# Performance work log

Hardware: AMD Instinct MI355X
Metric: run time of the kernel (lower is better)

Reference implementation:

```python
import jax, jax.numpy as jnp
import numpy as np

EPS = 1e-5

def _layernorm(x, g, b):
    mu = jnp.mean(x, axis=-1, keepdims=True)
    var = jnp.mean(jnp.square(x - mu), axis=-1, keepdims=True)
    return (x - mu) * jax.lax.rsqrt(var + EPS) * g + b

def _mlp(x, w1, b1, w2, b2):
    h = jax.nn.gelu(jnp.einsum('bnd,dh->bnh', x, w1) + b1, approximate=False)
    return jnp.einsum('bnh,hd->bnd', h, w2) + b2

def setup_inputs() -> dict:
    key = jax.random.key(0)
    B, N, D, H = 2, 8192, 1024, 4096
    ks = jax.random.split(key, 12)
    s1 = 1.0 / np.sqrt(D)
    s2 = 1.0 / np.sqrt(H)
    return {
        'x': jax.random.normal(ks[0], (B, N, D), dtype=jnp.float32),
        'mask': jax.random.randint(ks[1], (B, N), 0, 2) > 0,
        'g_rgb': jnp.ones((D,), jnp.float32),
        'b_rgb': jnp.zeros((D,), jnp.float32),
        'w1_rgb': jax.random.normal(ks[2], (D, H), dtype=jnp.float32) * s1,
        'b1_rgb': jnp.zeros((H,), jnp.float32),
        'w2_rgb': jax.random.normal(ks[3], (H, D), dtype=jnp.float32) * s2,
        'b2_rgb': jnp.zeros((D,), jnp.float32),
        'g_expr': jnp.ones((D,), jnp.float32),
        'b_expr': jnp.zeros((D,), jnp.float32),
        'w1_expr': jax.random.normal(ks[4], (D, H), dtype=jnp.float32) * s1,
        'b1_expr': jnp.zeros((H,), jnp.float32),
        'w2_expr': jax.random.normal(ks[5], (H, D), dtype=jnp.float32) * s2,
        'b2_expr': jnp.zeros((D,), jnp.float32),
    }

def reference(x, mask, g_rgb, b_rgb, w1_rgb, b1_rgb, w2_rgb, b2_rgb,
              g_expr, b_expr, w1_expr, b1_expr, w2_expr, b2_expr):
    # Per-token routing: rgb expert where mask, expr expert where ~mask.
    # LayerNorm+MLP are pointwise per token, so dense compute + select is
    # mathematically identical to the torch gather->compute->scatter.
    z_rgb = _mlp(_layernorm(x, g_rgb, b_rgb), w1_rgb, b1_rgb, w2_rgb, b2_rgb)
    z_expr = _mlp(_layernorm(x, g_expr, b_expr), w1_expr, b1_expr, w2_expr, b2_expr)
    z = jnp.where(mask[..., None], z_rgb, z_expr)
    return z.astype(jnp.float16)  # torch scatters into a float16 buffer
```

## Files before the change

kernel.cpp:

```cpp
#include <hip/hip_runtime.h>
#include <hip/hip_bf16.h>
#include <hip/hip_fp16.h>

#define D_ 1024
#define H_ 4096
#define NTOK 16384
#define MPAD 16640

typedef __attribute__((ext_vector_type(8))) short bf16x8;
typedef __attribute__((ext_vector_type(4))) float f32x4;

static __device__ __forceinline__ unsigned short f2bf(float f) {
  union { float f; unsigned u; } x; x.f = f;
  unsigned u = x.u + 0x7fffu + ((x.u >> 16) & 1u);
  return (unsigned short)(u >> 16);
}

static __device__ __forceinline__ void gld16(const void* g, void* l) {
  __builtin_amdgcn_global_load_lds(
      (const __attribute__((address_space(1))) unsigned int*)g,
      (__attribute__((address_space(3))) unsigned int*)l, 16, 0, 0);
}

static __device__ __forceinline__ float gelu_fast(float x) {
  const float z = x * (1.5957691216f + 0.0713548163f * x * x);
  return x * __builtin_amdgcn_rcpf(1.0f + __expf(-z));
}

__global__ __launch_bounds__(256) void transpose4_kernel(
    const float* __restrict__ w1r, const float* __restrict__ w1e,
    const float* __restrict__ w2r, const float* __restrict__ w2e,
    unsigned short* __restrict__ o1r, unsigned short* __restrict__ o1e,
    unsigned short* __restrict__ o2r, unsigned short* __restrict__ o2e) {
  __shared__ float tile[32][33];
  const int t = blockIdx.x;
  const float* src; unsigned short* dst; int R, C, tl;
  if (t < 4096)       { src = w1r; dst = o1r; R = D_; C = H_; tl = t; }
  else if (t < 8192)  { src = w1e; dst = o1e; R = D_; C = H_; tl = t - 4096; }
  else if (t < 12288) { src = w2r; dst = o2r; R = H_; C = D_; tl = t - 8192; }
  else                { src = w2e; dst = o2e; R = H_; C = D_; tl = t - 12288; }
  const int tc = C >> 5;
  const int r0 = (tl / tc) * 32, c0 = (tl % tc) * 32;
  const int tx = threadIdx.x & 31, ty = threadIdx.x >> 5;
#pragma unroll
  for (int i = 0; i < 32; i += 8)
    tile[ty + i][tx] = src[(size_t)(r0 + ty + i) * C + c0 + tx];
  __syncthreads();
#pragma unroll
  for (int i = 0; i < 32; i += 8)
    dst[(size_t)(c0 + ty + i) * R + r0 + tx] = f2bf(tile[tx][ty + i]);
}

__global__ __launch_bounds__(256) void compact_kernel(
    const int* __restrict__ mask, int* __restrict__ perm, int* __restrict__ counts) {
  const int NT = 256, CH = NTOK / NT;
  __shared__ int sm[NTOK];
  __shared__ int wsum[4];
  const int t = threadIdx.x;
  const int ln = t & 63, wv = t >> 6;
  for (int i = t; i < NTOK; i += NT) sm[i] = mask[i];
  for (int i = t; i < MPAD; i += NT) perm[i] = -1;
  __syncthreads();
  const int base = t * CH;
  int cnt = 0;
  for (int i = 0; i < CH; ++i) cnt += (sm[base + i] != 0);
  int sc = cnt;
#pragma unroll
  for (int o = 1; o < 64; o <<= 1) {
    int u = __shfl_up(sc, o, 64);
    if (ln >= o) sc += u;
  }
  if (ln == 63) wsum[wv] = sc;
  __syncthreads();
  int woff = 0;
#pragma unroll
  for (int j = 0; j < 4; ++j) woff += (j < wv) ? wsum[j] : 0;
  const int total1 = wsum[0] + wsum[1] + wsum[2] + wsum[3];
  if (t == 0) { counts[0] = total1; counts[1] = NTOK - total1; }
  const int excl = woff + sc - cnt;
  const int expr_base = ((total1 + 255) >> 8) << 8;
  int p1 = excl;
  int p0 = expr_base + (base - excl);
  for (int i = 0; i < CH; ++i) {
    const int idx = base + i;
    if (sm[idx] != 0) perm[p1++] = idx; else perm[p0++] = idx;
  }
}

__global__ __launch_bounds__(256) void ln_kernel(
    const float* __restrict__ x, const int* __restrict__ mask,
    const int* __restrict__ perm,
    const float* __restrict__ g_rgb, const float* __restrict__ b_rgb,
    const float* __restrict__ g_expr, const float* __restrict__ b_expr,
    unsigned short* __restrict__ xln) {
  const int i = blockIdx.x;
  const int t = perm[i];
  if (t < 0) return;
  const int tid = threadIdx.x;
  const float4 v = ((const float4*)(x + (size_t)t * D_))[tid];
  float s = v.x + v.y + v.z + v.w;
  float ss = v.x * v.x + v.y * v.y + v.z * v.z + v.w * v.w;
#pragma unroll
  for (int o = 32; o > 0; o >>= 1) {
    s += __shfl_xor(s, o, 64);
    ss += __shfl_xor(ss, o, 64);
  }
  __shared__ float red[8];
  const int wv = tid >> 6, ln = tid & 63;
  if (ln == 0) { red[wv] = s; red[4 + wv] = ss; }
  __syncthreads();
  s = red[0] + red[1] + red[2] + red[3];
  ss = red[4] + red[5] + red[6] + red[7];
  const float mu = s * (1.0f / D_);
  const float var = ss * (1.0f / D_) - mu * mu;
  const float rs = rsqrtf(var + 1e-5f);
  const bool rgb = mask[t] != 0;
  const float4 gv = ((const float4*)(rgb ? g_rgb : g_expr))[tid];
  const float4 bv = ((const float4*)(rgb ? b_rgb : b_expr))[tid];
  const unsigned short o0 = f2bf((v.x - mu) * rs * gv.x + bv.x);
  const unsigned short o1 = f2bf((v.y - mu) * rs * gv.y + bv.y);
  const unsigned short o2 = f2bf((v.z - mu) * rs * gv.z + bv.z);
  const unsigned short o3 = f2bf((v.w - mu) * rs * gv.w + bv.w);
  uint2 pk;
  pk.x = (unsigned)o0 | ((unsigned)o1 << 16);
  pk.y = (unsigned)o2 | ((unsigned)o3 << 16);
  *((uint2*)(xln + (size_t)i * D_ + tid * 4)) = pk;
}

template <int K, int N>
__global__ __launch_bounds__(512, 2) void gemm8_kernel(
    const unsigned short* __restrict__ A,
    const unsigned short* __restrict__ Wt_rgb,
    const unsigned short* __restrict__ Wt_expr,
    const float* __restrict__ bias_rgb,
    const float* __restrict__ bias_expr,
    const int* __restrict__ counts,
    unsigned short* __restrict__ Out) {
  constexpr int MT = MPAD / 256;
  constexpr int NT = N / 256;
  constexpr int ntk = K / 64;
  constexpr int KH2 = 128 * K * 2;

  const int tid = threadIdx.x;
  const int id = blockIdx.x;
  const int xcd = id & 7;
  const int slot = id >> 3;
  const int p = xcd * ((MT * NT) / 8) + slot;
  const int m0 = (p / NT) * 256;
  const int n0 = (p % NT) * 256;
  const int cnt_rgb = counts[0];
  const unsigned short* Wt = (m0 < cnt_rgb) ? Wt_rgb : Wt_expr;
  const float* bias = (m0 < cnt_rgb) ? bias_rgb : bias_expr;

  __shared__ unsigned short As[2][256 * 64];
  __shared__ unsigned short Bs[2][256 * 64];

  const int lane = tid & 63, wave = tid >> 6;
  const int wr = wave >> 2, wc = wave & 3;
  const int quad = lane >> 4, l16 = lane & 15;

  f32x4 acc[8][4] = {};

  const char* Abase = (const char*)A;
  const char* Wbase = (const char*)Wt;

  int agK0, agK1, bgK0, bgK1, sl0, sl1;
  {
    const int s0 = tid, s1 = 512 + tid;
    const int r0 = s0 >> 3, r1 = s1 >> 3;
    const int ks0 = ((s0 ^ r0) & 7) * 8, ks1 = ((s1 ^ r1) & 7) * 8;
    agK0 = ((m0 + r0) * K + ks0) * 2;  agK1 = ((m0 + r1) * K + ks1) * 2;
    bgK0 = ((n0 + r0) * K + ks0) * 2;  bgK1 = ((n0 + r1) * K + ks1) * 2;
    sl0 = s0 * 16;  sl1 = s1 * 16;
  }

  int aoffL[2][2][4];
  int boffL[2][4];
#pragma unroll
  for (int kk = 0; kk < 2; ++kk) {
    const int cb = kk * 4 + quad;
#pragma unroll
    for (int mh = 0; mh < 2; ++mh)
#pragma unroll
      for (int mi = 0; mi < 4; ++mi) {
        const int row = wr * 128 + mh * 64 + mi * 16 + l16;
        aoffL[kk][mh][mi] = (row * 64 + ((cb ^ row) & 7) * 8) * 2;
      }
#pragma unroll
    for (int ni = 0; ni < 4; ++ni) {
      const int row = wc * 64 + ni * 16 + l16;
      boffL[kk][ni] = (row * 64 + ((cb ^ row) & 7) * 8) * 2;
    }
  }

  bf16x8 a0, a1, a2, a3;
  bf16x8 bb[4];

#define STAGE_A(T1, HA, Q) do { \
    gld16(Abase + agK0 + (HA) * KH2 + (T1) * 128, (char*)As + (Q) * 32768 + (HA) * 16384 + sl0); \
    gld16(Abase + agK1 + (HA) * KH2 + (T1) * 128, (char*)As + (Q) * 32768 + (HA) * 16384 + sl1); \
  } while (0)
#define STAGE_B(T2, HB, Q) do { \
    gld16(Wbase + bgK0 + (HB) * KH2 + (T2) * 128, (char*)Bs + (Q) * 32768 + (HB) * 16384 + sl0); \
    gld16(Wbase + bgK1 + (HB) * KH2 + (T2) * 128, (char*)Bs + (Q) * 32768 + (HB) * 16384 + sl1); \
  } while (0)
#define RD_A(P_, KK, MH) do { \
    const char* _ab = (const char*)As + (P_) * 32768; \
    a0 = *(const bf16x8*)(_ab + aoffL[KK][MH][0]); \
    a1 = *(const bf16x8*)(_ab + aoffL[KK][MH][1]); \
    a2 = *(const bf16x8*)(_ab + aoffL[KK][MH][2]); \
    a3 = *(const bf16x8*)(_ab + aoffL[KK][MH][3]); \
  } while (0)
#define RD_B(P_, KK) do { \
    const char* _bp = (const char*)Bs + (P_) * 32768; \
    bb[0] = *(const bf16x8*)(_bp + boffL[KK][0]); \
    bb[1] = *(const bf16x8*)(_bp + boffL[KK][1]); \
    bb[2] = *(const bf16x8*)(_bp + boffL[KK][2]); \
    bb[3] = *(const bf16x8*)(_bp + boffL[KK][3]); \
  } while (0)
#define MFMA16(MO) do { \
    acc[(MO)+0][0] = __builtin_amdgcn_mfma_f32_16x16x32_bf16(a0, bb[0], acc[(MO)+0][0], 0, 0, 0); \
    acc[(MO)+0][1] = __builtin_amdgcn_mfma_f32_16x16x32_bf16(a0, bb[1], acc[(MO)+0][1], 0, 0, 0); \
    acc[(MO)+0][2] = __builtin_amdgcn_mfma_f32_16x16x32_bf16(a0, bb[2], acc[(MO)+0][2], 0, 0, 0); \
    acc[(MO)+0][3] = __builtin_amdgcn_mfma_f32_16x16x32_bf16(a0, bb[3], acc[(MO)+0][3], 0, 0, 0); \
    acc[(MO)+1][0] = __builtin_amdgcn_mfma_f32_16x16x32_bf16(a1, bb[0], acc[(MO)+1][0], 0, 0, 0); \
    acc[(MO)+1][1] = __builtin_amdgcn_mfma_f32_16x16x32_bf16(a1, bb[1], acc[(MO)+1][1], 0, 0, 0); \
    acc[(MO)+1][2] = __builtin_amdgcn_mfma_f32_16x16x32_bf16(a1, bb[2], acc[(MO)+1][2], 0, 0, 0); \
    acc[(MO)+1][3] = __builtin_amdgcn_mfma_f32_16x16x32_bf16(a1, bb[3], acc[(MO)+1][3], 0, 0, 0); \
    acc[(MO)+2][0] = __builtin_amdgcn_mfma_f32_16x16x32_bf16(a2, bb[0], acc[(MO)+2][0], 0, 0, 0); \
    acc[(MO)+2][1] = __builtin_amdgcn_mfma_f32_16x16x32_bf16(a2, bb[1], acc[(MO)+2][1], 0, 0, 0); \
    acc[(MO)+2][2] = __builtin_amdgcn_mfma_f32_16x16x32_bf16(a2, bb[2], acc[(MO)+2][2], 0, 0, 0); \
    acc[(MO)+2][3] = __builtin_amdgcn_mfma_f32_16x16x32_bf16(a2, bb[3], acc[(MO)+2][3], 0, 0, 0); \
    acc[(MO)+3][0] = __builtin_amdgcn_mfma_f32_16x16x32_bf16(a3, bb[0], acc[(MO)+3][0], 0, 0, 0); \
    acc[(MO)+3][1] = __builtin_amdgcn_mfma_f32_16x16x32_bf16(a3, bb[1], acc[(MO)+3][1], 0, 0, 0); \
    acc[(MO)+3][2] = __builtin_amdgcn_mfma_f32_16x16x32_bf16(a3, bb[2], acc[(MO)+3][2], 0, 0, 0); \
    acc[(MO)+3][3] = __builtin_amdgcn_mfma_f32_16x16x32_bf16(a3, bb[3], acc[(MO)+3][3], 0, 0, 0); \
  } while (0)

#define KTILE(T_, P_, SA_, SB_, VMC_) do { \
     \
    RD_B(P_, 0); RD_A(P_, 0, 0); \
    if (SA_) STAGE_A((T_) + 1, 0, (P_) ^ 1); \
    __builtin_amdgcn_s_barrier(); \
    __builtin_amdgcn_s_setprio(1); MFMA16(0); __builtin_amdgcn_s_setprio(0); \
    __builtin_amdgcn_s_barrier(); \
     \
    RD_A(P_, 0, 1); \
    if (SA_) STAGE_A((T_) + 1, 1, (P_) ^ 1); \
    __builtin_amdgcn_s_barrier(); \
    __builtin_amdgcn_s_setprio(1); MFMA16(4); __builtin_amdgcn_s_setprio(0); \
    __builtin_amdgcn_s_barrier(); \
     \
    RD_B(P_, 1); RD_A(P_, 1, 0); \
    __builtin_amdgcn_s_barrier(); \
    __builtin_amdgcn_s_setprio(1); MFMA16(0); __builtin_amdgcn_s_setprio(0); \
    __builtin_amdgcn_s_barrier(); \
     \
    RD_A(P_, 1, 1); \
    if (SB_) { STAGE_B((T_) + 2, 0, P_); STAGE_B((T_) + 2, 1, P_); } \
    __builtin_amdgcn_s_barrier(); \
    __builtin_amdgcn_s_setprio(1); MFMA16(4); __builtin_amdgcn_s_setprio(0); \
    if ((VMC_) == 4) { asm volatile("s_waitcnt vmcnt(4)" ::: "memory"); } \
    else if ((VMC_) == 0) { asm volatile("s_waitcnt vmcnt(0)" ::: "memory"); } \
    __builtin_amdgcn_sched_barrier(0); \
    __builtin_amdgcn_s_barrier(); \
  } while (0)

  STAGE_A(0, 0, 0); STAGE_A(0, 1, 0);
  STAGE_B(0, 0, 0); STAGE_B(0, 1, 0);
  STAGE_B(1, 0, 1); STAGE_B(1, 1, 1);
  asm volatile("s_waitcnt vmcnt(4)" ::: "memory");
  __builtin_amdgcn_sched_barrier(0);
  __builtin_amdgcn_s_barrier();

  for (int tt = 0; tt < ntk / 2 - 1; ++tt) {
    const int t0 = tt * 2;
    KTILE(t0, 0, 1, 1, 4);
    KTILE(t0 + 1, 1, 1, 1, 4);
  }
  KTILE(ntk - 2, 0, 1, 0, 0);
  KTILE(ntk - 1, 1, 0, 0, -1);

#undef KTILE
#undef MFMA16
#undef RD_B
#undef RD_A
#undef STAGE_B
#undef STAGE_A

  float bv[4];
#pragma unroll
  for (int ni = 0; ni < 4; ++ni) bv[ni] = bias[n0 + wc * 64 + ni * 16 + l16];
#pragma unroll
  for (int mi = 0; mi < 8; ++mi) {
#pragma unroll
    for (int r = 0; r < 4; ++r) {
      const int row = m0 + wr * 128 + mi * 16 + quad * 4 + r;
      unsigned short* orow = Out + (size_t)row * N + n0 + wc * 64 + l16;
#pragma unroll
      for (int ni = 0; ni < 4; ++ni)
        orow[ni * 16] = f2bf(gelu_fast(acc[mi][ni][r] + bv[ni]));
    }
  }
}

template <int EP, int K, int N>
__global__ __launch_bounds__(256) void gemm_kernel(
    const unsigned short* __restrict__ A,
    const unsigned short* __restrict__ Wt_rgb,
    const unsigned short* __restrict__ Wt_expr,
    const float* __restrict__ bias_rgb,
    const float* __restrict__ bias_expr,
    const int* __restrict__ counts,
    const int* __restrict__ perm,
    void* __restrict__ OutP) {
  constexpr int BM = 128, BN = 128, BK = 64;
  constexpr int MT = MPAD / BM;
  constexpr int NT = N / BN;
  const int tid = threadIdx.x;
  const int id = blockIdx.x;
  const int xcd = id & 7;
  const int slot = id >> 3;
  const int p = xcd * ((MT * NT) / 8) + slot;
  const int m0 = (p / NT) * BM;
  const int n0 = (p % NT) * BN;
  const int cnt_rgb = counts[0];
  const unsigned short* Wt = (m0 < cnt_rgb) ? Wt_rgb : Wt_expr;
  const float* bias = (m0 < cnt_rgb) ? bias_rgb : bias_expr;

  __shared__ unsigned short As[BM * BK];
  __shared__ unsigned short Bs[BN * BK];

  f32x4 acc[4][4] = {};

  const int lane = tid & 63, wave = tid >> 6;
  const int wm = (wave & 1) * 64, wn = (wave >> 1) * 64;
  const int quad = lane >> 4, l16 = lane & 15;

  const char* Abase = (const char*)A;
  const char* Wbase = (const char*)Wt;
  const char* AsB = (const char*)As;
  const char* BsB = (const char*)Bs;

  int ag[4], bg[4], sl[4];
#pragma unroll
  for (int it = 0; it < 4; ++it) {
    const int s = it * 256 + tid;
    const int row = s >> 3;
    const int ks = ((s ^ row) & 7) * 8;
    ag[it] = ((m0 + row) * K + ks) * 2;
    bg[it] = ((n0 + row) * K + ks) * 2;
    sl[it] = s * 16;
  }
  int aoff[2][4], boff[2][4];
#pragma unroll
  for (int hh = 0; hh < 2; ++hh) {
    const int cb = hh * 4 + quad;
#pragma unroll
    for (int mi = 0; mi < 4; ++mi) {
      const int row = wm + mi * 16 + l16;
      aoff[hh][mi] = (row * BK + (((cb ^ row) & 7) << 3)) * 2;
    }
#pragma unroll
    for (int ni = 0; ni < 4; ++ni) {
      const int row = wn + ni * 16 + l16;
      boff[hh][ni] = (row * BK + (((cb ^ row) & 7) << 3)) * 2;
    }
  }

  for (int k0 = 0; k0 < K; k0 += BK) {
#pragma unroll
    for (int it = 0; it < 4; ++it) {
      gld16(Abase + ag[it], (void*)(AsB + sl[it]));
      gld16(Wbase + bg[it], (void*)(BsB + sl[it]));
      ag[it] += BK * 2;
      bg[it] += BK * 2;
    }
    __syncthreads();
#pragma unroll
    for (int hh = 0; hh < 2; ++hh) {
      bf16x8 a[4], b[4];
#pragma unroll
      for (int mi = 0; mi < 4; ++mi) a[mi] = *(const bf16x8*)(AsB + aoff[hh][mi]);
#pragma unroll
      for (int ni = 0; ni < 4; ++ni) b[ni] = *(const bf16x8*)(BsB + boff[hh][ni]);
#pragma unroll
      for (int mi = 0; mi < 4; ++mi)
#pragma unroll
        for (int ni = 0; ni < 4; ++ni)
          acc[mi][ni] = __builtin_amdgcn_mfma_f32_16x16x32_bf16(a[mi], b[ni], acc[mi][ni], 0, 0, 0);
    }
    __syncthreads();
  }

  float bv[4];
#pragma unroll
  for (int ni = 0; ni < 4; ++ni) bv[ni] = bias[n0 + wn + ni * 16 + l16];

#pragma unroll
  for (int mi = 0; mi < 4; ++mi) {
#pragma unroll
    for (int r = 0; r < 4; ++r) {
      const int row = m0 + wm + mi * 16 + quad * 4 + r;
      if (EP == 0) {
        unsigned short* orow = (unsigned short*)OutP + (size_t)row * N + n0 + wn + l16;
#pragma unroll
        for (int ni = 0; ni < 4; ++ni) {
          orow[ni * 16] = f2bf(gelu_fast(acc[mi][ni][r] + bv[ni]));
        }
      } else {
        const int p2 = perm[row];
        if (p2 < 0) continue;
        float* orow = (float*)OutP + (size_t)p2 * N + n0 + wn + l16;
#pragma unroll
        for (int ni = 0; ni < 4; ++ni) {
          float v = acc[mi][ni][r] + bv[ni];
          orow[ni * 16] = __half2float(__float2half_rn(v));
        }
      }
    }
  }
}

extern "C" void kernel_launch(void* const* d_in, const int* in_sizes, int n_in,
                              void* d_out, int out_size, void* d_ws, size_t ws_size,
                              hipStream_t stream) {
  const float* x       = (const float*)d_in[0];
  const int*   mask    = (const int*)d_in[1];
  const float* g_rgb   = (const float*)d_in[2];
  const float* b_rgb   = (const float*)d_in[3];
  const float* w1_rgb  = (const float*)d_in[4];
  const float* b1_rgb  = (const float*)d_in[5];
  const float* w2_rgb  = (const float*)d_in[6];
  const float* b2_rgb  = (const float*)d_in[7];
  const float* g_expr  = (const float*)d_in[8];
  const float* b_expr  = (const float*)d_in[9];
  const float* w1_expr = (const float*)d_in[10];
  const float* b1_expr = (const float*)d_in[11];
  const float* w2_expr = (const float*)d_in[12];
  const float* b2_expr = (const float*)d_in[13];

  char* w = (char*)d_ws;
  int* counts               = (int*)(w + 0);
  int* perm                 = (int*)(w + 256);
  unsigned short* w1t_rgb   = (unsigned short*)(w + 66816);
  unsigned short* w1t_expr  = (unsigned short*)(w + 8455424);
  unsigned short* w2t_rgb   = (unsigned short*)(w + 16844032);
  unsigned short* w2t_expr  = (unsigned short*)(w + 25232640);
  unsigned short* xln       = (unsigned short*)(w + 33621248);
  unsigned short* h         = (unsigned short*)(w + 67699968);

  compact_kernel<<<1, 256, 0, stream>>>(mask, perm, counts);

  transpose4_kernel<<<16384, 256, 0, stream>>>(
      w1_rgb, w1_expr, w2_rgb, w2_expr, w1t_rgb, w1t_expr, w2t_rgb, w2t_expr);

  ln_kernel<<<MPAD, 256, 0, stream>>>(x, mask, perm, g_rgb, b_rgb, g_expr, b_expr, xln);

  gemm8_kernel<D_, H_><<<dim3((MPAD / 256) * (H_ / 256)), 512, 0, stream>>>(
      xln, w1t_rgb, w1t_expr, b1_rgb, b1_expr, counts, h);

  gemm_kernel<1, H_, D_><<<dim3((D_ / 128) * (MPAD / 128)), 256, 0, stream>>>(
      h, w2t_rgb, w2t_expr, b2_rgb, b2_expr, counts, perm, d_out);
}
```

Measured before the change: 574.6 us.

## Triple-buffer A tiles in LDS to prefetch two k-steps ahead

Adds a third LDS buffer for the A operand so A tiles are prefetched two k-steps ahead instead of one, matching the B prefetch depth. The main loop becomes a 6-tile rotation over the A and B buffers with deeper vmcnt waits, and the tail is adjusted for the new schedule. The aim is to hide more global-load latency. It raises LDS use to 160KB per block, which may limit occupancy to one block per CU despite launch_bounds(512,2).

```diff
diff --git a/kernel.cpp b/kernel.cpp
--- a/kernel.cpp
+++ b/kernel.cpp
@@ -139,6 +139,7 @@
   constexpr int MT = MPAD / 256;
   constexpr int NT = N / 256;
   constexpr int ntk = K / 64;
+  static_assert(ntk >= 10 && (ntk - 4) % 6 == 0, "tail pattern needs ntk = 6m+4");
   constexpr int KH2 = 128 * K * 2;
 
   const int tid = threadIdx.x;
@@ -152,7 +153,7 @@
   const unsigned short* Wt = (m0 < cnt_rgb) ? Wt_rgb : Wt_expr;
   const float* bias = (m0 < cnt_rgb) ? bias_rgb : bias_expr;
 
-  __shared__ unsigned short As[2][256 * 64];
+  __shared__ unsigned short As[3][256 * 64];
   __shared__ unsigned short Bs[2][256 * 64];
 
   const int lane = tid & 63, wave = tid >> 6;
@@ -204,15 +205,15 @@
     gld16(Wbase + bgK0 + (HB) * KH2 + (T2) * 128, (char*)Bs + (Q) * 32768 + (HB) * 16384 + sl0); \
     gld16(Wbase + bgK1 + (HB) * KH2 + (T2) * 128, (char*)Bs + (Q) * 32768 + (HB) * 16384 + sl1); \
   } while (0)
-#define RD_A(P_, KK, MH) do { \
-    const char* _ab = (const char*)As + (P_) * 32768; \
+#define RD_A(Q_, KK, MH) do { \
+    const char* _ab = (const char*)As + (Q_) * 32768; \
     a0 = *(const bf16x8*)(_ab + aoffL[KK][MH][0]); \
     a1 = *(const bf16x8*)(_ab + aoffL[KK][MH][1]); \
     a2 = *(const bf16x8*)(_ab + aoffL[KK][MH][2]); \
     a3 = *(const bf16x8*)(_ab + aoffL[KK][MH][3]); \
   } while (0)
-#define RD_B(P_, KK) do { \
-    const char* _bp = (const char*)Bs + (P_) * 32768; \
+#define RD_B(Q_, KK) do { \
+    const char* _bp = (const char*)Bs + (Q_) * 32768; \
     bb[0] = *(const bf16x8*)(_bp + boffL[KK][0]); \
     bb[1] = *(const bf16x8*)(_bp + boffL[KK][1]); \
     bb[2] = *(const bf16x8*)(_bp + boffL[KK][2]); \
@@ -237,30 +238,30 @@
     acc[(MO)+3][3] = __builtin_amdgcn_mfma_f32_16x16x32_bf16(a3, bb[3], acc[(MO)+3][3], 0, 0, 0); \
   } while (0)
 
-#define KTILE(T_, P_, SA_, SB_, VMC_) do { \
+#define KTILE(T_, AQ_, AQN_, BQ_, SA_, SB_, VMC_) do { \
      \
-    RD_B(P_, 0); RD_A(P_, 0, 0); \
-    if (SA_) STAGE_A((T_) + 1, 0, (P_) ^ 1); \
+    RD_B(BQ_, 0); RD_A(AQ_, 0, 0); \
+    if (SA_) STAGE_A((T_) + 2, 0, AQN_); \
     __builtin_amdgcn_s_barrier(); \
     __builtin_amdgcn_s_setprio(1); MFMA16(0); __builtin_amdgcn_s_setprio(0); \
     __builtin_amdgcn_s_barrier(); \
      \
-    RD_A(P_, 0, 1); \
-    if (SA_) STAGE_A((T_) + 1, 1, (P_) ^ 1); \
+    RD_A(AQ_, 0, 1); \
+    if (SA_) STAGE_A((T_) + 2, 1, AQN_); \
     __builtin_amdgcn_s_barrier(); \
     __builtin_amdgcn_s_setprio(1); MFMA16(4); __builtin_amdgcn_s_setprio(0); \
     __builtin_amdgcn_s_barrier(); \
      \
-    RD_B(P_, 1); RD_A(P_, 1, 0); \
+    RD_B(BQ_, 1); RD_A(AQ_, 1, 0); \
     __builtin_amdgcn_s_barrier(); \
     __builtin_amdgcn_s_setprio(1); MFMA16(0); __builtin_amdgcn_s_setprio(0); \
     __builtin_amdgcn_s_barrier(); \
      \
-    RD_A(P_, 1, 1); \
-    if (SB_) { STAGE_B((T_) + 2, 0, P_); STAGE_B((T_) + 2, 1, P_); } \
+    RD_A(AQ_, 1, 1); \
+    if (SB_) { STAGE_B((T_) + 2, 0, BQ_); STAGE_B((T_) + 2, 1, BQ_); } \
     __builtin_amdgcn_s_barrier(); \
     __builtin_amdgcn_s_setprio(1); MFMA16(4); __builtin_amdgcn_s_setprio(0); \
-    if ((VMC_) == 4) { asm volatile("s_waitcnt vmcnt(4)" ::: "memory"); } \
+    if ((VMC_) == 8) { asm volatile("s_waitcnt vmcnt(8)" ::: "memory"); } \
     else if ((VMC_) == 0) { asm volatile("s_waitcnt vmcnt(0)" ::: "memory"); } \
     __builtin_amdgcn_sched_barrier(0); \
     __builtin_amdgcn_s_barrier(); \
@@ -268,18 +269,24 @@
 
   STAGE_A(0, 0, 0); STAGE_A(0, 1, 0);
   STAGE_B(0, 0, 0); STAGE_B(0, 1, 0);
+  STAGE_A(1, 0, 1); STAGE_A(1, 1, 1);
   STAGE_B(1, 0, 1); STAGE_B(1, 1, 1);
-  asm volatile("s_waitcnt vmcnt(4)" ::: "memory");
+  asm volatile("s_waitcnt vmcnt(8)" ::: "memory");
   __builtin_amdgcn_sched_barrier(0);
   __builtin_amdgcn_s_barrier();
 
-  for (int tt = 0; tt < ntk / 2 - 1; ++tt) {
-    const int t0 = tt * 2;
-    KTILE(t0, 0, 1, 1, 4);
-    KTILE(t0 + 1, 1, 1, 1, 4);
-  }
-  KTILE(ntk - 2, 0, 1, 0, 0);
-  KTILE(ntk - 1, 1, 0, 0, -1);
+  for (int t6 = 0; t6 < ntk - 4; t6 += 6) {
+    KTILE(t6 + 0, 0, 2, 0, 1, 1, 8);
+    KTILE(t6 + 1, 1, 0, 1, 1, 1, 8);
+    KTILE(t6 + 2, 2, 1, 0, 1, 1, 8);
+    KTILE(t6 + 3, 0, 2, 1, 1, 1, 8);
+    KTILE(t6 + 4, 1, 0, 0, 1, 1, 8);
+    KTILE(t6 + 5, 2, 1, 1, 1, 1, 8);
+  }
+  KTILE(ntk - 4, 0, 2, 0, 1, 1, 8);
+  KTILE(ntk - 3, 1, 0, 1, 1, 1, 8);
+  KTILE(ntk - 2, 2, 1, 0, 0, 0, 0);
+  KTILE(ntk - 1, 0, 2, 1, 0, 0, -1);
 
 #undef KTILE
 #undef MFMA16
```

Result: no change. 580.9 us (+1.1%).
